# Kernel tuning notes

Measured on AMD Instinct MI355X. Metric: run time of the kernel, lower is better.

The kernel has to match this reference:

```python
import jax, jax.numpy as jnp
import numpy as np

DIM = 1024
HEADS = 16
HEAD_DIM = 64
INNER = HEADS * HEAD_DIM  # 1024
B, N = 4, 2048
EPS = 1e-5


def setup_inputs() -> dict:
    key = jax.random.key(0)
    ks = jax.random.split(key, 5)
    x = jax.random.normal(ks[0], (B, N, DIM), dtype=jnp.float32)
    w_qkv = jax.random.normal(ks[1], (DIM, 3 * INNER), dtype=jnp.float32) * (DIM ** -0.5)
    w_out = jax.random.normal(ks[2], (INNER, DIM), dtype=jnp.float32) * (INNER ** -0.5)
    b_out = jax.random.normal(ks[3], (DIM,), dtype=jnp.float32) * 0.01
    ln_gamma = jnp.ones((DIM,), dtype=jnp.float32)
    ln_beta = jnp.zeros((DIM,), dtype=jnp.float32)
    return {"x": x, "w_qkv": w_qkv, "w_out": w_out, "b_out": b_out,
            "ln_gamma": ln_gamma, "ln_beta": ln_beta}


def reference(x, w_qkv, w_out, b_out, ln_gamma, ln_beta):
    scale = HEAD_DIM ** -0.5
    qkv = x @ w_qkv  # [b, n, 3*inner]
    q, k, v = jnp.split(qkv, 3, axis=-1)
    q = q * scale
    # [b, n, h*d] -> [b, h, n, d]
    def to_heads(t):
        b, n, _ = t.shape
        return t.reshape(b, n, HEADS, HEAD_DIM).transpose(0, 2, 1, 3)
    q, k, v = to_heads(q), to_heads(k), to_heads(v)
    scores = jnp.einsum('bhid,bhjd->bhij', q, k)
    attn = jax.nn.softmax(scores, axis=-1)  # max-subtraction (detached) is internal
    out = jnp.einsum('bhij,bhjd->bhid', attn, v)
    out = out.transpose(0, 2, 1, 3).reshape(x.shape[0], x.shape[1], INNER)
    out = out @ w_out + b_out
    # LayerNorm over last dim
    mu = out.mean(axis=-1, keepdims=True)
    var = out.var(axis=-1, keepdims=True)
    out = (out - mu) * jax.lax.rsqrt(var + EPS)
    return out * ln_gamma + ln_beta
```

## Files before the change

### kernel.cpp

```cpp
#include <hip/hip_runtime.h>


typedef __bf16 bf16;
typedef __bf16 bf16x4 __attribute__((ext_vector_type(4)));
typedef __bf16 bf16x8 __attribute__((ext_vector_type(8)));
typedef float f32x4 __attribute__((ext_vector_type(4)));
typedef float f32x16 __attribute__((ext_vector_type(16)));
typedef unsigned int u32x2 __attribute__((ext_vector_type(2)));
typedef unsigned int u32x4 __attribute__((ext_vector_type(4)));

#define QSCALE_LOG2E 0.18033688011112042f

#define GLOAD_LDS16(gp, lp)                                                   \
  __builtin_amdgcn_global_load_lds(                                           \
      (const __attribute__((address_space(1))) unsigned int*)(const void*)(gp), \
      (__attribute__((address_space(3))) unsigned int*)(void*)(lp), 16, 0, 0)

__device__ __forceinline__ float fexp2(float x) {
#if __has_builtin(__builtin_amdgcn_exp2f)
  return __builtin_amdgcn_exp2f(x);
#else
  return __expf(x * 0.6931471805599453f);
#endif
}

__device__ __forceinline__ unsigned pack2t(float lo, float hi) {
  return __builtin_amdgcn_perm(__float_as_uint(hi), __float_as_uint(lo), 0x07060302u);
}

__global__ __launch_bounds__(256) void cvt_k(const float* __restrict__ in,
                                             bf16* __restrict__ out) {
  const size_t i = ((size_t)blockIdx.x * 256 + threadIdx.x) * 8;
  float4 a = *(const float4*)(in + i);
  float4 b = *(const float4*)(in + i + 4);
  bf16x8 o = {(bf16)a.x, (bf16)a.y, (bf16)a.z, (bf16)a.w,
              (bf16)b.x, (bf16)b.y, (bf16)b.z, (bf16)b.w};
  *(bf16x8*)(out + i) = o;
}

__global__ __launch_bounds__(256) void transpose_k(const float* __restrict__ in,
                                                   bf16* __restrict__ out,
                                                   int Kd, int Nd) {
  __shared__ bf16 t[32][36];
  const int n0 = blockIdx.x * 32, k0 = blockIdx.y * 32;
  const int r = threadIdx.x >> 3, c4 = (threadIdx.x & 7) * 4;
  float4 v = *(const float4*)(in + (size_t)(k0 + r) * Nd + n0 + c4);
  t[c4 + 0][r] = (bf16)v.x; t[c4 + 1][r] = (bf16)v.y;
  t[c4 + 2][r] = (bf16)v.z; t[c4 + 3][r] = (bf16)v.w;
  __syncthreads();
  bf16x4 o = *(const bf16x4*)&t[r][c4];
  *(bf16x4*)(out + (size_t)(n0 + r) * Kd + k0 + c4) = o;
}

template <bool QKV>
__global__ __launch_bounds__(256) void gemm2(const bf16* __restrict__ A,
                                             const bf16* __restrict__ Bt,
                                             bf16* __restrict__ C,
                                             bf16* __restrict__ Vt) {
  __shared__ bf16 As[128][32];
  __shared__ bf16 Bs[128][32];
  const int tid = threadIdx.x;
  const int l = tid & 63, w = tid >> 6;
  const int g = l >> 4, q = l & 15;
  const int wm = w >> 1, wn = w & 1;
  const int m0 = blockIdx.x * 128, n0 = blockIdx.y * 128;
  const int lr = l >> 2, lc = (l & 3) * 8;

  f32x4 acc[4][4] = {};

  for (int k0 = 0; k0 < 1024; k0 += 32) {
    __syncthreads();
#pragma unroll
    for (int i = 0; i < 2; i++) {
      const int c = w + i * 4;
      GLOAD_LDS16(A + (size_t)(m0 + c * 16 + lr) * 1024 + k0 + lc, &As[c * 16][0]);
      GLOAD_LDS16(Bt + (size_t)(n0 + c * 16 + lr) * 1024 + k0 + lc, &Bs[c * 16][0]);
    }
    __syncthreads();

    bf16x8 af[4], bfr[4];
#pragma unroll
    for (int mi = 0; mi < 4; mi++)
      af[mi] = *(const bf16x8*)&As[wm * 64 + mi * 16 + q][g * 8];
#pragma unroll
    for (int ni = 0; ni < 4; ni++)
      bfr[ni] = *(const bf16x8*)&Bs[wn * 64 + ni * 16 + q][g * 8];
#pragma unroll
    for (int mi = 0; mi < 4; mi++)
#pragma unroll
      for (int ni = 0; ni < 4; ni++)
        acc[mi][ni] = __builtin_amdgcn_mfma_f32_16x16x32_bf16(af[mi], bfr[ni], acc[mi][ni], 0, 0, 0);
  }

  if (QKV && n0 >= 2048) {
#pragma unroll
    for (int mi = 0; mi < 4; mi++)
#pragma unroll
      for (int ni = 0; ni < 4; ni++) {
        const int vcol = n0 - 2048 + wn * 64 + ni * 16 + q;
        const int h = vcol >> 6, d = vcol & 63;
        const int t0 = m0 + wm * 64 + mi * 16 + g * 4;
        const int b = t0 >> 11, n = t0 & 2047;
        bf16x4 o = {(bf16)acc[mi][ni][0], (bf16)acc[mi][ni][1],
                    (bf16)acc[mi][ni][2], (bf16)acc[mi][ni][3]};
        *(bf16x4*)(Vt + ((size_t)(b * 16 + h) * 64 + d) * 2048 + n) = o;
      }
  } else {
    const int ldc = QKV ? 2048 : 1024;
    const float s = (QKV && n0 < 1024) ? QSCALE_LOG2E : 1.0f;
#pragma unroll
    for (int mi = 0; mi < 4; mi++)
#pragma unroll
      for (int ni = 0; ni < 4; ni++) {
        const int col = n0 + wn * 64 + ni * 16 + q;
#pragma unroll
        for (int r = 0; r < 4; r++) {
          const int row = m0 + wm * 64 + mi * 16 + g * 4 + r;
          C[(size_t)row * ldc + col] = (bf16)(acc[mi][ni][r] * s);
        }
      }
  }
}

__global__ __launch_bounds__(256, 3) void attn_k(const bf16* __restrict__ qk,
                                                 const bf16* __restrict__ vt,
                                                 bf16* __restrict__ aout) {
  __shared__ bf16 Ks[3][64][64];
  __shared__ bf16 Vs[3][64][64];
  const int tid = threadIdx.x;
  const int l = tid & 63, w = tid >> 6;
  const int q = l & 31, hi = l >> 5, q7 = q & 7;

  const int flat = blockIdx.x;
  const int logical = (flat & 7) * 128 + (flat >> 3);
  const int qt = logical & 15, bh = logical >> 4;
  const int h = bh & 15, b = bh >> 4;
  const int qbase = qt * 128 + w * 32;

  const bf16* Kg = qk + (size_t)(b * 2048) * 2048 + 1024 + h * 64;
  const bf16* Vg = vt + ((size_t)(b * 16 + h) * 64) * 2048;

  bf16x8 qf[4];
  {
    const bf16* Qr = qk + (size_t)(b * 2048 + qbase + q) * 2048 + h * 64 + hi * 8;
#pragma unroll
    for (int i = 0; i < 4; i++) qf[i] = *(const bf16x8*)(Qr + i * 16);
  }

  const int r0 = tid >> 3, sp0 = ((tid & 7) ^ (r0 & 7)) * 8;
  const int ub = (tid >> 6) << 9;
#define STAGE_KV(buf, kt)                                                       \
  do {                                                                          \
    bf16* kd = &Ks[buf][0][0];                                                  \
    bf16* vd = &Vs[buf][0][0];                                                  \
    GLOAD_LDS16(Kg + (size_t)((kt) + r0) * 2048 + sp0, kd + ub);                \
    GLOAD_LDS16(Vg + (size_t)r0 * 2048 + (kt) + sp0, vd + ub);                  \
    GLOAD_LDS16(Kg + (size_t)((kt) + 32 + r0) * 2048 + sp0, kd + 2048 + ub);    \
    GLOAD_LDS16(Vg + (size_t)(32 + r0) * 2048 + (kt) + sp0, vd + 2048 + ub);    \
  } while (0)

#define QKT(buf, sA, sB)                                                        \
  do {                                                                          \
    const char* Kb_ = (const char*)&Ks[buf][0][0];                              \
    __builtin_amdgcn_s_setprio(1);                                              \
    {                                                                           \
      f32x16 a_ = {};                                                           \
      _Pragma("unroll")                                                         \
      for (int i = 0; i < 4; i++) {                                             \
        bf16x8 kf = *(const bf16x8*)(Kb_ + q * 128 + (((2 * i + hi) ^ q7) << 4));\
        a_ = __builtin_amdgcn_mfma_f32_32x32x16_bf16(kf, qf[i], a_, 0, 0, 0);   \
      }                                                                         \
      sA = a_;                                                                  \
    }                                                                           \
    {                                                                           \
      f32x16 a_ = {};                                                           \
      _Pragma("unroll")                                                         \
      for (int i = 0; i < 4; i++) {                                             \
        bf16x8 kf = *(const bf16x8*)(Kb_ + (32 + q) * 128 +                     \
                                     (((2 * i + hi) ^ q7) << 4));               \
        a_ = __builtin_amdgcn_mfma_f32_32x32x16_bf16(kf, qf[i], a_, 0, 0, 0);   \
      }                                                                         \
      sB = a_;                                                                  \
    }                                                                           \
    __builtin_amdgcn_s_setprio(0);                                              \
  } while (0)

  f32x16 oacc[2] = {};
  float lsA = 0.f, lsB = 0.f;

  STAGE_KV(0, 0);
  STAGE_KV(1, 64);
  asm volatile("s_waitcnt vmcnt(4)" ::: "memory");
  __builtin_amdgcn_sched_barrier(0);
  __builtin_amdgcn_s_barrier();

  f32x16 s0, s1;
  QKT(0, s0, s1);

  int cur = 0;
  for (int kt = 0; kt < 2048; kt += 64) {
    const int nbuf = (cur == 2) ? 0 : cur + 1;
    const int sbuf = (nbuf == 2) ? 0 : nbuf + 1;

    asm volatile("s_waitcnt vmcnt(0)" ::: "memory");
    __builtin_amdgcn_sched_barrier(0);
    __builtin_amdgcn_s_barrier();

    if (kt + 128 < 2048) STAGE_KV(sbuf, kt + 128);

    f32x16 n0v, n1v;
    QKT(nbuf, n0v, n1v);

#pragma unroll
    for (int r = 0; r < 16; r++) { s0[r] = fexp2(s0[r]); lsA += s0[r]; }
#pragma unroll
    for (int r = 0; r < 16; r++) { s1[r] = fexp2(s1[r]); lsB += s1[r]; }

    bf16x8 pfrag[4];
#pragma unroll
    for (int ks = 0; ks < 2; ks++) {
      const unsigned a0 = pack2t(s0[8 * ks + 0], s0[8 * ks + 1]);
      const unsigned a1 = pack2t(s0[8 * ks + 2], s0[8 * ks + 3]);
      const unsigned b0 = pack2t(s0[8 * ks + 4], s0[8 * ks + 5]);
      const unsigned b1 = pack2t(s0[8 * ks + 6], s0[8 * ks + 7]);
      u32x2 w0 = __builtin_amdgcn_permlane32_swap(a0, b0, false, false);
      u32x2 w1 = __builtin_amdgcn_permlane32_swap(a1, b1, false, false);
      u32x4 bw = {w0[0], w1[0], w0[1], w1[1]};
      pfrag[ks] = __builtin_bit_cast(bf16x8, bw);
    }
#pragma unroll
    for (int ks = 0; ks < 2; ks++) {
      const unsigned a0 = pack2t(s1[8 * ks + 0], s1[8 * ks + 1]);
      const unsigned a1 = pack2t(s1[8 * ks + 2], s1[8 * ks + 3]);
      const unsigned b0 = pack2t(s1[8 * ks + 4], s1[8 * ks + 5]);
      const unsigned b1 = pack2t(s1[8 * ks + 6], s1[8 * ks + 7]);
      u32x2 w0 = __builtin_amdgcn_permlane32_swap(a0, b0, false, false);
      u32x2 w1 = __builtin_amdgcn_permlane32_swap(a1, b1, false, false);
      u32x4 bw = {w0[0], w1[0], w0[1], w1[1]};
      pfrag[2 + ks] = __builtin_bit_cast(bf16x8, bw);
    }

    const char* Vb = (const char*)&Vs[cur][0][0];
    __builtin_amdgcn_s_setprio(1);
#pragma unroll
    for (int dblk = 0; dblk < 2; dblk++) {
      bf16x8 vfr[4];
#pragma unroll
      for (int t = 0; t < 4; t++)
        vfr[t] = *(const bf16x8*)(Vb + (dblk * 32 + q) * 128 + (((2 * t + hi) ^ q7) << 4));
#pragma unroll
      for (int t = 0; t < 4; t++)
        oacc[dblk] = __builtin_amdgcn_mfma_f32_32x32x16_bf16(vfr[t], pfrag[t],
                                                             oacc[dblk], 0, 0, 0);
    }
    __builtin_amdgcn_s_setprio(0);

    s0 = n0v; s1 = n1v;
    cur = nbuf;
  }

  float lsum = lsA + lsB;
  {
    u32x2 t2 = __builtin_amdgcn_permlane32_swap(__float_as_uint(lsum),
                                                __float_as_uint(lsum), false, false);
    lsum = __uint_as_float(t2[0]) + __uint_as_float(t2[1]);
  }
  const float inv = 1.f / lsum;
  bf16* orow = aout + (size_t)(b * 2048 + qbase + q) * 1024 + h * 64 + hi * 4;
#pragma unroll
  for (int dblk = 0; dblk < 2; dblk++)
#pragma unroll
    for (int rg = 0; rg < 4; rg++) {
      bf16x4 o = {(bf16)(oacc[dblk][4 * rg + 0] * inv), (bf16)(oacc[dblk][4 * rg + 1] * inv),
                  (bf16)(oacc[dblk][4 * rg + 2] * inv), (bf16)(oacc[dblk][4 * rg + 3] * inv)};
      *(bf16x4*)(orow + dblk * 32 + rg * 8) = o;
    }
#undef QKT
#undef STAGE_KV
}

__global__ __launch_bounds__(256) void ln_k(const bf16* __restrict__ proj,
                                            const float* __restrict__ bo,
                                            const float* __restrict__ gam,
                                            const float* __restrict__ bet,
                                            float* __restrict__ out) {
  const int row = blockIdx.x, tid = threadIdx.x;
  const int l = tid & 63, w = tid >> 6;
  bf16x4 pv = *(const bf16x4*)(proj + (size_t)row * 1024 + tid * 4);
  float4 bv = *(const float4*)(bo + tid * 4);
  float v0 = (float)pv[0] + bv.x, v1 = (float)pv[1] + bv.y;
  float v2 = (float)pv[2] + bv.z, v3 = (float)pv[3] + bv.w;
  float s = v0 + v1 + v2 + v3;
  float ss = v0 * v0 + v1 * v1 + v2 * v2 + v3 * v3;
#pragma unroll
  for (int off = 32; off > 0; off >>= 1) {
    s += __shfl_xor(s, off);
    ss += __shfl_xor(ss, off);
  }
  __shared__ float red[8];
  if (l == 0) { red[w] = s; red[w + 4] = ss; }
  __syncthreads();
  const float S = red[0] + red[1] + red[2] + red[3];
  const float SS = red[4] + red[5] + red[6] + red[7];
  const float mean = S * (1.f / 1024.f);
  const float var = SS * (1.f / 1024.f) - mean * mean;
  const float rs = rsqrtf(var + 1e-5f);
  float4 gv = *(const float4*)(gam + tid * 4);
  float4 btv = *(const float4*)(bet + tid * 4);
  float4 o;
  o.x = (v0 - mean) * rs * gv.x + btv.x;
  o.y = (v1 - mean) * rs * gv.y + btv.y;
  o.z = (v2 - mean) * rs * gv.z + btv.z;
  o.w = (v3 - mean) * rs * gv.w + btv.w;
  *(float4*)(out + (size_t)row * 1024 + tid * 4) = o;
}

extern "C" void kernel_launch(void* const* d_in, const int* in_sizes, int n_in,
                              void* d_out, int out_size, void* d_ws, size_t ws_size,
                              hipStream_t stream) {
  const float* x      = (const float*)d_in[0];
  const float* w_qkv  = (const float*)d_in[1];
  const float* w_out  = (const float*)d_in[2];
  const float* b_out  = (const float*)d_in[3];
  const float* gamma  = (const float*)d_in[4];
  const float* beta   = (const float*)d_in[5];
  float* out = (float*)d_out;

  char* ws = (char*)d_ws;
  bf16* xbf   = (bf16*)(ws);
  bf16* wqkvT = (bf16*)(ws + 16777216);
  bf16* woutT = (bf16*)(ws + 23068672);
  bf16* qkbuf = (bf16*)(ws + 25165824);
  bf16* vt    = (bf16*)(ws + 58720256);
  bf16* aout  = xbf;
  bf16* proj  = vt;

  dim3 blk(256);
  cvt_k<<<4096, blk, 0, stream>>>(x, xbf);
  transpose_k<<<dim3(96, 32), blk, 0, stream>>>(w_qkv, wqkvT, 1024, 3072);
  transpose_k<<<dim3(32, 32), blk, 0, stream>>>(w_out, woutT, 1024, 1024);
  gemm2<true><<<dim3(64, 24), blk, 0, stream>>>(xbf, wqkvT, qkbuf, vt);
  attn_k<<<1024, blk, 0, stream>>>(qkbuf, vt, aout);
  gemm2<false><<<dim3(64, 8), blk, 0, stream>>>(aout, woutT, proj, nullptr);
  ln_k<<<8192, blk, 0, stream>>>(proj, b_out, gamma, beta, out);
}
```

Baseline: 200.5 us.

## Double GEMM K-tile with XOR-swizzled LDS and one-wave-per-row LayerNorm

The GEMM now stages 64-wide K tiles instead of 32, which halves the number of sync/load iterations. Each tile is stored in LDS with an XOR swizzle on the 16-byte chunk index so that the MFMA fragment reads avoid bank conflicts. The LayerNorm kernel now handles one row per wavefront with 16 elements per lane, so only shuffle reductions are needed and no shared memory or barrier, with a quarter as many blocks. The trade-off is that LDS usage doubles per block, which may lower occupancy.

```diff
diff --git a/kernel.cpp b/kernel.cpp
--- a/kernel.cpp
+++ b/kernel.cpp
@@ -57,39 +57,51 @@
                                              const bf16* __restrict__ Bt,
                                              bf16* __restrict__ C,
                                              bf16* __restrict__ Vt) {
-  __shared__ bf16 As[128][32];
-  __shared__ bf16 Bs[128][32];
+  __shared__ bf16 As[128][64];
+  __shared__ bf16 Bs[128][64];
   const int tid = threadIdx.x;
   const int l = tid & 63, w = tid >> 6;
-  const int g = l >> 4, q = l & 15;
+  const int g = l >> 4, q = l & 15, q7 = q & 7;
   const int wm = w >> 1, wn = w & 1;
   const int m0 = blockIdx.x * 128, n0 = blockIdx.y * 128;
-  const int lr = l >> 2, lc = (l & 3) * 8;
+  const int lr = tid >> 3;
+  const int sc = ((tid & 7) ^ (lr & 7)) * 8;
 
   f32x4 acc[4][4] = {};
 
-  for (int k0 = 0; k0 < 1024; k0 += 32) {
+  for (int k0 = 0; k0 < 1024; k0 += 64) {
     __syncthreads();
 #pragma unroll
-    for (int i = 0; i < 2; i++) {
-      const int c = w + i * 4;
-      GLOAD_LDS16(A + (size_t)(m0 + c * 16 + lr) * 1024 + k0 + lc, &As[c * 16][0]);
-      GLOAD_LDS16(Bt + (size_t)(n0 + c * 16 + lr) * 1024 + k0 + lc, &Bs[c * 16][0]);
+    for (int k = 0; k < 4; k++) {
+      GLOAD_LDS16(A + (size_t)(m0 + lr + k * 32) * 1024 + k0 + sc,
+                  &As[0][0] + tid * 8 + k * 2048);
+      GLOAD_LDS16(Bt + (size_t)(n0 + lr + k * 32) * 1024 + k0 + sc,
+                  &Bs[0][0] + tid * 8 + k * 2048);
     }
     __syncthreads();
 
-    bf16x8 af[4], bfr[4];
-#pragma unroll
-    for (int mi = 0; mi < 4; mi++)
-      af[mi] = *(const bf16x8*)&As[wm * 64 + mi * 16 + q][g * 8];
-#pragma unroll
-    for (int ni = 0; ni < 4; ni++)
-      bfr[ni] = *(const bf16x8*)&Bs[wn * 64 + ni * 16 + q][g * 8];
-#pragma unroll
-    for (int mi = 0; mi < 4; mi++)
-#pragma unroll
-      for (int ni = 0; ni < 4; ni++)
-        acc[mi][ni] = __builtin_amdgcn_mfma_f32_16x16x32_bf16(af[mi], bfr[ni], acc[mi][ni], 0, 0, 0);
+#pragma unroll
+    for (int ks = 0; ks < 2; ks++) {
+      bf16x8 af[4], bfr[4];
+#pragma unroll
+      for (int mi = 0; mi < 4; mi++) {
+        const int R = wm * 64 + mi * 16 + q;
+        af[mi] = *(const bf16x8*)((const char*)&As[0][0] + R * 128 +
+                                  (((ks * 4 + g) ^ q7) << 4));
+      }
+#pragma unroll
+      for (int ni = 0; ni < 4; ni++) {
+        const int R = wn * 64 + ni * 16 + q;
+        bfr[ni] = *(const bf16x8*)((const char*)&Bs[0][0] + R * 128 +
+                                   (((ks * 4 + g) ^ q7) << 4));
+      }
+#pragma unroll
+      for (int mi = 0; mi < 4; mi++)
+#pragma unroll
+        for (int ni = 0; ni < 4; ni++)
+          acc[mi][ni] = __builtin_amdgcn_mfma_f32_16x16x32_bf16(af[mi], bfr[ni],
+                                                                acc[mi][ni], 0, 0, 0);
+    }
   }
 
   if (QKV && n0 >= 2048) {
@@ -284,35 +296,44 @@
                                             const float* __restrict__ gam,
                                             const float* __restrict__ bet,
                                             float* __restrict__ out) {
-  const int row = blockIdx.x, tid = threadIdx.x;
+  const int tid = threadIdx.x;
   const int l = tid & 63, w = tid >> 6;
-  bf16x4 pv = *(const bf16x4*)(proj + (size_t)row * 1024 + tid * 4);
-  float4 bv = *(const float4*)(bo + tid * 4);
-  float v0 = (float)pv[0] + bv.x, v1 = (float)pv[1] + bv.y;
-  float v2 = (float)pv[2] + bv.z, v3 = (float)pv[3] + bv.w;
-  float s = v0 + v1 + v2 + v3;
-  float ss = v0 * v0 + v1 * v1 + v2 * v2 + v3 * v3;
+  const int row = blockIdx.x * 4 + w;
+  const int c0 = l * 16;
+
+  bf16x8 p0 = *(const bf16x8*)(proj + (size_t)row * 1024 + c0);
+  bf16x8 p1 = *(const bf16x8*)(proj + (size_t)row * 1024 + c0 + 8);
+  float v[16];
+#pragma unroll
+  for (int j = 0; j < 8; j++) { v[j] = (float)p0[j]; v[8 + j] = (float)p1[j]; }
+#pragma unroll
+  for (int j = 0; j < 4; j++) {
+    float4 bv = *(const float4*)(bo + c0 + j * 4);
+    v[4 * j + 0] += bv.x; v[4 * j + 1] += bv.y;
+    v[4 * j + 2] += bv.z; v[4 * j + 3] += bv.w;
+  }
+  float s = 0.f, ss = 0.f;
+#pragma unroll
+  for (int j = 0; j < 16; j++) { s += v[j]; ss += v[j] * v[j]; }
 #pragma unroll
   for (int off = 32; off > 0; off >>= 1) {
     s += __shfl_xor(s, off);
     ss += __shfl_xor(ss, off);
   }
-  __shared__ float red[8];
-  if (l == 0) { red[w] = s; red[w + 4] = ss; }
-  __syncthreads();
-  const float S = red[0] + red[1] + red[2] + red[3];
-  const float SS = red[4] + red[5] + red[6] + red[7];
-  const float mean = S * (1.f / 1024.f);
-  const float var = SS * (1.f / 1024.f) - mean * mean;
+  const float mean = s * (1.f / 1024.f);
+  const float var = ss * (1.f / 1024.f) - mean * mean;
   const float rs = rsqrtf(var + 1e-5f);
-  float4 gv = *(const float4*)(gam + tid * 4);
-  float4 btv = *(const float4*)(bet + tid * 4);
-  float4 o;
-  o.x = (v0 - mean) * rs * gv.x + btv.x;
-  o.y = (v1 - mean) * rs * gv.y + btv.y;
-  o.z = (v2 - mean) * rs * gv.z + btv.z;
-  o.w = (v3 - mean) * rs * gv.w + btv.w;
-  *(float4*)(out + (size_t)row * 1024 + tid * 4) = o;
+#pragma unroll
+  for (int j = 0; j < 4; j++) {
+    float4 gv = *(const float4*)(gam + c0 + j * 4);
+    float4 btv = *(const float4*)(bet + c0 + j * 4);
+    float4 o;
+    o.x = (v[4 * j + 0] - mean) * rs * gv.x + btv.x;
+    o.y = (v[4 * j + 1] - mean) * rs * gv.y + btv.y;
+    o.z = (v[4 * j + 2] - mean) * rs * gv.z + btv.z;
+    o.w = (v[4 * j + 3] - mean) * rs * gv.w + btv.w;
+    *(float4*)(out + (size_t)row * 1024 + c0 + j * 4) = o;
+  }
 }
 
 extern "C" void kernel_launch(void* const* d_in, const int* in_sizes, int n_in,
@@ -342,5 +363,5 @@
   gemm2<true><<<dim3(64, 24), blk, 0, stream>>>(xbf, wqkvT, qkbuf, vt);
   attn_k<<<1024, blk, 0, stream>>>(qkbuf, vt, aout);
   gemm2<false><<<dim3(64, 8), blk, 0, stream>>>(aout, woutT, proj, nullptr);
-  ln_k<<<8192, blk, 0, stream>>>(proj, b_out, gamma, beta, out);
-}
+  ln_k<<<2048, blk, 0, stream>>>(proj, b_out, gamma, beta, out);
+}
```

Result: slower. 205.5 us (+2.5%).
